# Performance work log

Hardware: AMD Instinct MI355X
Metric: run time of the kernel (lower is better)

The kernel has to match this reference:

```python
import jax, jax.numpy as jnp
import numpy as np

DIM = 1024
NUM_HEADS = 16
MASKED = True


def setup_inputs() -> dict:
    key = jax.random.key(0)
    ks = jax.random.split(key, 9)
    B, S, D = 2, 2048, DIM
    return {
        "x": jax.random.normal(ks[0], (B, S, D), dtype=jnp.float32),
        "Wq": jax.random.normal(ks[1], (D, D), dtype=jnp.float32),
        "bq": jax.random.normal(ks[2], (D,), dtype=jnp.float32),
        "Wk": jax.random.normal(ks[3], (D, D), dtype=jnp.float32),
        "bk": jax.random.normal(ks[4], (D,), dtype=jnp.float32),
        "Wv": jax.random.normal(ks[5], (D, D), dtype=jnp.float32),
        "bv": jax.random.normal(ks[6], (D,), dtype=jnp.float32),
        "Wo": jax.random.normal(ks[7], (D, D), dtype=jnp.float32),
        "bo": jax.random.normal(ks[8], (D,), dtype=jnp.float32),
    }


def _mha(x, Wq, bq, Wk, bk, Wv, bv, Wo, bo):
    B, S, D = x.shape
    H = NUM_HEADS
    hd = D // H
    # projections (torch Linear stores [out,in]; here W is [out,in], x @ W.T + b)
    q = x @ Wq.T + bq
    k = x @ Wk.T + bk
    v = x @ Wv.T + bv
    # [B, H, S, hd]
    q = q.reshape(B, S, H, hd).transpose(0, 2, 1, 3)
    k = k.reshape(B, S, H, hd).transpose(0, 2, 1, 3)
    v = v.reshape(B, S, H, hd).transpose(0, 2, 1, 3)
    scores = jnp.einsum("bhqd,bhkd->bhqk", q, k) / jnp.sqrt(jnp.asarray(hd, x.dtype))
    if MASKED:
        mask = jnp.tril(jnp.ones((S, S), dtype=bool))
        scores = jnp.where(mask, scores, -jnp.inf)
    attn = jax.nn.softmax(scores, axis=-1)
    out = jnp.einsum("bhqk,bhkd->bhqd", attn, v)
    out = out.transpose(0, 2, 1, 3).reshape(B, S, D)
    return out @ Wo.T + bo


def reference(x, Wq, bq, Wk, bk, Wv, bv, Wo, bo):
    return _mha(x, Wq, bq, Wk, bk, Wv, bv, Wo, bo)
```

## Files before the change

### kernel.cpp

```cpp
#include <hip/hip_runtime.h>

typedef unsigned short u16;
typedef unsigned int u32;
typedef __attribute__((ext_vector_type(4))) float f32x4;
typedef __attribute__((ext_vector_type(8))) __bf16 bf16x8;

#define L2E 1.4426950408889634f

__device__ __forceinline__ u16 f2bf(float f) { return __builtin_bit_cast(u16, (__bf16)f); }
__device__ __forceinline__ float bf2f(u16 h) { return (float)__builtin_bit_cast(__bf16, h); }
__device__ __forceinline__ f32x4 mfma16(bf16x8 a, bf16x8 b, f32x4 c) {
  return __builtin_amdgcn_mfma_f32_16x16x32_bf16(a, b, c, 0, 0, 0);
}
__device__ __forceinline__ void gl_lds16(const u16* g, u16* l) {
  __builtin_amdgcn_global_load_lds((__attribute__((address_space(1))) void*)g,
                                   (__attribute__((address_space(3))) void*)l,
                                   16, 0, 0);
}
__device__ __forceinline__ f32x4 fzero() {
  f32x4 v = {0.f, 0.f, 0.f, 0.f};
  return v;
}

__global__ void k_prep(const float* __restrict__ x, const float* __restrict__ Wq,
                       const float* __restrict__ Wk, const float* __restrict__ Wv,
                       const float* __restrict__ Wo,
                       u16* __restrict__ xh, u16* __restrict__ xl,
                       u16* __restrict__ wqh, u16* __restrict__ wql,
                       u16* __restrict__ wkh, u16* __restrict__ wkl,
                       u16* __restrict__ wvb, u16* __restrict__ wob) {
  int i = (blockIdx.x * 256 + threadIdx.x) * 4;
  const float* src;
  u16* hi;
  u16* lo;
  int j;
  if (i < 4194304)      { src = x;  hi = xh;  lo = xl;      j = i; }
  else if (i < 5242880) { src = Wq; hi = wqh; lo = wql;     j = i - 4194304; }
  else if (i < 6291456) { src = Wk; hi = wkh; lo = wkl;     j = i - 5242880; }
  else if (i < 7340032) { src = Wv; hi = wvb; lo = nullptr; j = i - 6291456; }
  else                  { src = Wo; hi = wob; lo = nullptr; j = i - 7340032; }
  float4 v = *(const float4*)(src + j);
  float vv[4] = {v.x, v.y, v.z, v.w};
  u16 hh[4];
#pragma unroll
  for (int t = 0; t < 4; ++t) hh[t] = f2bf(vv[t]);
  *(ushort4*)(hi + j) = make_ushort4(hh[0], hh[1], hh[2], hh[3]);
  if (lo) {
    u16 ll[4];
#pragma unroll
    for (int t = 0; t < 4; ++t) ll[t] = f2bf(vv[t] - bf2f(hh[t]));
    *(ushort4*)(lo + j) = make_ushort4(ll[0], ll[1], ll[2], ll[3]);
  }
}

template <int SPLIT, int EPI>
__device__ __forceinline__ void gemm_body(
    u16* sm, const u16* __restrict__ Ah, const u16* __restrict__ Al,
    const u16* __restrict__ Bh, const u16* __restrict__ Bl,
    const float* __restrict__ bias, float scale,
    u16* __restrict__ oH, u16* __restrict__ oL, float* __restrict__ oF,
    int m0, int n0) {
  u16* sAh = sm;
  u16* sBh = sm + 4096;
  u16* sAl = SPLIT ? (sm + 8192) : sm;
  u16* sBl = SPLIT ? (sm + 12288) : sm;

  const int tid = threadIdx.x;
  const int lane = tid & 63, w = tid >> 6;
  const int wm = w >> 1, wn = w & 1;
  const int fr = lane & 15, fg = lane >> 4;
  const int srow = tid >> 2, sblk = tid & 3;
  const int sswz = (sblk ^ (srow & 3)) * 8;
  const int sdst = sblk * 8;
  const int rswz = (fg ^ (fr & 3)) * 8;

  f32x4 acc[4][4];
#pragma unroll
  for (int i = 0; i < 4; ++i)
#pragma unroll
    for (int j = 0; j < 4; ++j) acc[i][j] = fzero();

  for (int kk = 0; kk < 1024; kk += 32) {
    __syncthreads();
#pragma unroll
    for (int r = 0; r < 2; ++r) {
      int row = r * 64 + srow;
      gl_lds16(Ah + (size_t)(m0 + row) * 1024 + kk + sswz, sAh + row * 32 + sdst);
      gl_lds16(Bh + (size_t)(n0 + row) * 1024 + kk + sswz, sBh + row * 32 + sdst);
      if constexpr (SPLIT) {
        gl_lds16(Al + (size_t)(m0 + row) * 1024 + kk + sswz, sAl + row * 32 + sdst);
        gl_lds16(Bl + (size_t)(n0 + row) * 1024 + kk + sswz, sBl + row * 32 + sdst);
      }
    }
    __syncthreads();

    bf16x8 ah[4], bh[4], al[4], bl[4];
#pragma unroll
    for (int i = 0; i < 4; ++i) {
      ah[i] = *(const bf16x8*)(sAh + (wm * 64 + i * 16 + fr) * 32 + rswz);
      bh[i] = *(const bf16x8*)(sBh + (wn * 64 + i * 16 + fr) * 32 + rswz);
      if constexpr (SPLIT) {
        al[i] = *(const bf16x8*)(sAl + (wm * 64 + i * 16 + fr) * 32 + rswz);
        bl[i] = *(const bf16x8*)(sBl + (wn * 64 + i * 16 + fr) * 32 + rswz);
      }
    }
#pragma unroll
    for (int i = 0; i < 4; ++i)
#pragma unroll
      for (int j = 0; j < 4; ++j) {
        acc[i][j] = mfma16(ah[i], bh[j], acc[i][j]);
        if constexpr (SPLIT) {
          acc[i][j] = mfma16(ah[i], bl[j], acc[i][j]);
          acc[i][j] = mfma16(al[i], bh[j], acc[i][j]);
        }
      }
  }

#pragma unroll
  for (int i = 0; i < 4; ++i)
#pragma unroll
    for (int j = 0; j < 4; ++j) {
      int cg = n0 + wn * 64 + j * 16 + fr;
      float bv = bias[cg];
      if constexpr (EPI == 1) {
        int rgb = m0 + wm * 64 + i * 16 + fg * 4;
        int b = rgb >> 11, s = rgb & 2047, hd2 = cg >> 6, dd = cg & 63;
        u16 hv[4];
#pragma unroll
        for (int r = 0; r < 4; ++r) hv[r] = f2bf((acc[i][j][r] + bv) * scale);
        *(ushort4*)(oH + ((size_t)((b * 16 + hd2) * 64 + dd)) * 2048 + s) =
            make_ushort4(hv[0], hv[1], hv[2], hv[3]);
      } else {
#pragma unroll
        for (int r = 0; r < 4; ++r) {
          int rg = m0 + wm * 64 + i * 16 + fg * 4 + r;
          float val = (acc[i][j][r] + bv) * scale;
          if constexpr (EPI == 0) {
            int b = rg >> 11, s = rg & 2047, hd2 = cg >> 6, dd = cg & 63;
            size_t off = ((size_t)((b * 16 + hd2) * 2048 + s)) * 64 + dd;
            u16 hv = f2bf(val);
            oH[off] = hv;
            oL[off] = f2bf(val - bf2f(hv));
          } else {
            oF[(size_t)rg * 1024 + cg] = val;
          }
        }
      }
    }
}

__global__ __launch_bounds__(256) void k_qkv(
    const u16* __restrict__ xh, const u16* __restrict__ xl,
    const u16* __restrict__ wqh, const u16* __restrict__ wql,
    const u16* __restrict__ wkh, const u16* __restrict__ wkl,
    const u16* __restrict__ wvb,
    const float* __restrict__ bq, const float* __restrict__ bk,
    const float* __restrict__ bv,
    u16* __restrict__ qh, u16* __restrict__ ql,
    u16* __restrict__ kh, u16* __restrict__ kl, u16* __restrict__ vt) {
  __shared__ u16 sm[16384];
  int which = blockIdx.y >> 3;
  int m0 = blockIdx.x * 128, n0 = (blockIdx.y & 7) * 128;
  if (which == 0)
    gemm_body<1, 0>(sm, xh, xl, wqh, wql, bq, 0.125f * L2E, qh, ql, nullptr, m0, n0);
  else if (which == 1)
    gemm_body<1, 0>(sm, xh, xl, wkh, wkl, bk, 1.0f, kh, kl, nullptr, m0, n0);
  else
    gemm_body<0, 1>(sm, xh, nullptr, wvb, nullptr, bv, 1.0f, vt, nullptr, nullptr, m0, n0);
}

__global__ __launch_bounds__(256) void k_oproj(
    const u16* __restrict__ A, const u16* __restrict__ B,
    const float* __restrict__ bias, float* __restrict__ out) {
  __shared__ u16 sm[6144];
  u16* sA = sm;
  u16* sB = sm + 2048;

  const int tid = threadIdx.x;
  const int lane = tid & 63, w = tid >> 6;
  const int fr = lane & 15, fg = lane >> 4;
  const int m0 = blockIdx.x * 64, n0 = blockIdx.y * 128;
  const int srow = tid >> 2, sblk = tid & 3;
  const int sswz = (sblk ^ (srow & 3)) * 8;
  const int sdst = sblk * 8;
  const int rswz = (fg ^ (fr & 3)) * 8;

  f32x4 acc[4][2];
#pragma unroll
  for (int i = 0; i < 4; ++i)
#pragma unroll
    for (int j = 0; j < 2; ++j) acc[i][j] = fzero();

  for (int kk = 0; kk < 1024; kk += 32) {
    __syncthreads();
    gl_lds16(A + (size_t)(m0 + srow) * 1024 + kk + sswz, sA + srow * 32 + sdst);
    gl_lds16(B + (size_t)(n0 + srow) * 1024 + kk + sswz, sB + srow * 32 + sdst);
    gl_lds16(B + (size_t)(n0 + 64 + srow) * 1024 + kk + sswz, sB + (64 + srow) * 32 + sdst);
    __syncthreads();

    bf16x8 af[4], bf_[2];
#pragma unroll
    for (int i = 0; i < 4; ++i)
      af[i] = *(const bf16x8*)(sA + (i * 16 + fr) * 32 + rswz);
#pragma unroll
    for (int j = 0; j < 2; ++j)
      bf_[j] = *(const bf16x8*)(sB + (w * 32 + j * 16 + fr) * 32 + rswz);
#pragma unroll
    for (int i = 0; i < 4; ++i)
#pragma unroll
      for (int j = 0; j < 2; ++j) acc[i][j] = mfma16(af[i], bf_[j], acc[i][j]);
  }

#pragma unroll
  for (int i = 0; i < 4; ++i)
#pragma unroll
    for (int j = 0; j < 2; ++j) {
      int cg = n0 + w * 32 + j * 16 + fr;
      float bv = bias[cg];
#pragma unroll
      for (int r = 0; r < 4; ++r) {
        int rg = m0 + i * 16 + fg * 4 + r;
        out[(size_t)rg * 1024 + cg] = acc[i][j][r] + bv;
      }
    }
}

__global__ __launch_bounds__(512) void k_attn(
    const u16* __restrict__ Qh, const u16* __restrict__ Ql,
    const u16* __restrict__ Kh, const u16* __restrict__ Kl,
    const u16* __restrict__ Vt, u16* __restrict__ Oa) {
  __shared__ u16 sKh[2][4096], sKl[2][4096], sVt[2][4096];
  __shared__ u16 sP[8][1024];

  const int tid = threadIdx.x;
  const int lane = tid & 63, w = tid >> 6;
  const int fr = lane & 15, fg = lane >> 4;

  const int d = blockIdx.x;
  const int g = d >> 3;
  const int bh = (d & 7) * 4 + (g & 3);
  const int pr = g >> 2;

  const size_t base = (size_t)bh * 131072;
  const u16* Qh_p = Qh + base;
  const u16* Ql_p = Ql + base;
  const u16* Kh_p = Kh + base;
  const u16* Kl_p = Kl + base;
  const u16* Vt_p = Vt + base;
  const int bb = bh >> 4, hh = bh & 15;

  const int srow8 = tid >> 3, scb8 = tid & 7;

  auto STAGE = [&](int t, int c) {
    int cbs = scb8 ^ (srow8 & 7);
    gl_lds16(Kh_p + ((size_t)(t * 64 + srow8)) * 64 + cbs * 8, &sKh[c][srow8 * 64 + scb8 * 8]);
    gl_lds16(Kl_p + ((size_t)(t * 64 + srow8)) * 64 + cbs * 8, &sKl[c][srow8 * 64 + scb8 * 8]);
    gl_lds16(Vt_p + (size_t)srow8 * 2048 + t * 64 + cbs * 8, &sVt[c][srow8 * 64 + scb8 * 8]);
  };

  for (int half = 0; half < 2; ++half) {
    const int j = half ? (15 - pr) : pr;
    const int nt = 2 * (j + 1);
    const int qrow = j * 128 + w * 16 + fr;

    bf16x8 qhf[2], qlf[2];
#pragma unroll
    for (int ks = 0; ks < 2; ++ks) {
      qhf[ks] = *(const bf16x8*)(Qh_p + (size_t)qrow * 64 + ks * 32 + fg * 8);
      qlf[ks] = *(const bf16x8*)(Ql_p + (size_t)qrow * 64 + ks * 32 + fg * 8);
    }

    float mx = -1e30f, l = 0.f;
    f32x4 o[4];
#pragma unroll
    for (int f = 0; f < 4; ++f) o[f] = fzero();

    STAGE(0, 0);

    for (int t = 0; t < nt; ++t) {
      const int cur = t & 1;
      if (t + 1 < nt) {
        STAGE(t + 1, cur ^ 1);
        asm volatile("s_waitcnt vmcnt(3)" ::: "memory");
      } else {
        asm volatile("s_waitcnt vmcnt(0)" ::: "memory");
      }
      asm volatile("s_barrier" ::: "memory");

      const u16* kbh = sKh[cur];
      const u16* kbl = sKl[cur];
      const u16* vbb = sVt[cur];

      f32x4 sc[4];
      __builtin_amdgcn_s_setprio(1);
#pragma unroll
      for (int f = 0; f < 4; ++f) {
        f32x4 a = fzero();
#pragma unroll
        for (int ks = 0; ks < 2; ++ks) {
          int row = f * 16 + fr;
          int cb = (fg + 4 * ks) ^ (fr & 7);
          bf16x8 khv = *(const bf16x8*)(kbh + row * 64 + cb * 8);
          bf16x8 klv = *(const bf16x8*)(kbl + row * 64 + cb * 8);
          a = mfma16(khv, qhf[ks], a);
          a = mfma16(khv, qlf[ks], a);
          a = mfma16(klv, qhf[ks], a);
        }
        sc[f] = a;
      }
      __builtin_amdgcn_s_setprio(0);

      if (t >= nt - 2) {
#pragma unroll
        for (int f = 0; f < 4; ++f)
#pragma unroll
          for (int r = 0; r < 4; ++r) {
            int kvg = t * 64 + f * 16 + fg * 4 + r;
            if (kvg > qrow) sc[f][r] = -1e30f;
          }
      }

      float pm = -1e30f;
#pragma unroll
      for (int f = 0; f < 4; ++f)
#pragma unroll
        for (int r = 0; r < 4; ++r) pm = fmaxf(pm, sc[f][r]);
      pm = fmaxf(pm, __shfl_xor(pm, 16, 64));
      pm = fmaxf(pm, __shfl_xor(pm, 32, 64));

      const bool resc = __any(pm > mx + 11.5f);
      float alp = 1.0f;
      if (resc) {
        float mn = fmaxf(mx, pm);
        alp = exp2f(mx - mn);
        mx = mn;
      }

      float ps = 0.f;
#pragma unroll
      for (int f = 0; f < 4; ++f) {
        float p0 = exp2f(sc[f][0] - mx);
        float p1 = exp2f(sc[f][1] - mx);
        float p2 = exp2f(sc[f][2] - mx);
        float p3 = exp2f(sc[f][3] - mx);
        ps += (p0 + p1) + (p2 + p3);
        uint2 pv;
        pv.x = (u32)f2bf(p0) | ((u32)f2bf(p1) << 16);
        pv.y = (u32)f2bf(p2) | ((u32)f2bf(p3) << 16);
        int e = (f * 16 + fg * 4) ^ ((fr & 7) << 3);
        *(uint2*)(&sP[w][fr * 64 + e]) = pv;
      }
      ps += __shfl_xor(ps, 16, 64);
      ps += __shfl_xor(ps, 32, 64);
      l = l * alp + ps;

      if (resc) {
        float alpb[4];
#pragma unroll
        for (int r = 0; r < 4; ++r) alpb[r] = __shfl(alp, fg * 4 + r, 64);
#pragma unroll
        for (int f = 0; f < 4; ++f)
#pragma unroll
          for (int r = 0; r < 4; ++r) o[f][r] *= alpb[r];
      }

      __builtin_amdgcn_s_setprio(1);
#pragma unroll
      for (int ks = 0; ks < 2; ++ks) {
        int e = (ks * 32 + fg * 8) ^ ((fr & 7) << 3);
        bf16x8 pa = *(const bf16x8*)(&sP[w][fr * 64 + e]);
#pragma unroll
        for (int f = 0; f < 4; ++f) {
          int row = f * 16 + fr;
          int cb = (fg + 4 * ks) ^ (fr & 7);
          bf16x8 vb = *(const bf16x8*)(vbb + row * 64 + cb * 8);
          o[f] = mfma16(pa, vb, o[f]);
        }
      }
      __builtin_amdgcn_s_setprio(0);

      asm volatile("s_barrier" ::: "memory");
    }

    float lb[4];
#pragma unroll
    for (int r = 0; r < 4; ++r) lb[r] = __shfl(l, fg * 4 + r, 64);
#pragma unroll
    for (int f = 0; f < 4; ++f)
#pragma unroll
      for (int r = 0; r < 4; ++r) {
        int qg = j * 128 + w * 16 + fg * 4 + r;
        float val = o[f][r] / lb[r];
        Oa[((size_t)(bb * 2048 + qg)) * 1024 + hh * 64 + f * 16 + fr] = f2bf(val);
      }
  }
}

extern "C" void kernel_launch(void* const* d_in, const int* in_sizes, int n_in,
                              void* d_out, int out_size, void* d_ws, size_t ws_size,
                              hipStream_t stream) {
  const float* x  = (const float*)d_in[0];
  const float* Wq = (const float*)d_in[1];
  const float* bq = (const float*)d_in[2];
  const float* Wk = (const float*)d_in[3];
  const float* bk = (const float*)d_in[4];
  const float* Wv = (const float*)d_in[5];
  const float* bv = (const float*)d_in[6];
  const float* Wo = (const float*)d_in[7];
  const float* bo = (const float*)d_in[8];
  float* out = (float*)d_out;

  u16* ws  = (u16*)d_ws;
  u16* xh  = ws;
  u16* xl  = xh + 4194304;
  u16* wqh = xl + 4194304;
  u16* wql = wqh + 1048576;
  u16* wkh = wql + 1048576;
  u16* wkl = wkh + 1048576;
  u16* wvb = wkl + 1048576;
  u16* wob = wvb + 1048576;
  u16* qh  = wob + 1048576;
  u16* ql  = qh + 4194304;
  u16* kh  = ql + 4194304;
  u16* kl  = kh + 4194304;
  u16* vt  = kl + 4194304;
  u16* ao  = xh;

  k_prep<<<8192, 256, 0, stream>>>(x, Wq, Wk, Wv, Wo, xh, xl, wqh, wql, wkh, wkl, wvb, wob);
  k_qkv<<<dim3(32, 24), 256, 0, stream>>>(xh, xl, wqh, wql, wkh, wkl, wvb, bq, bk, bv,
                                          qh, ql, kh, kl, vt);
  k_attn<<<256, 512, 0, stream>>>(qh, ql, kh, kl, vt, ao);
  k_oproj<<<dim3(64, 8), 256, 0, stream>>>(ao, wob, bo, out);
}
```

Before: 173.3 us.

## Double GEMM K-tile, remap QKV blocks per XCD, triple-buffer attention K/V

The QKV and output-projection GEMMs now stage 64-wide K tiles with a new XOR swizzle, which halves the barrier count per K. They also raise MFMA priority and add occupancy hints to launch_bounds. The QKV grid becomes 1D, with block indices remapped so blocks on the same XCD share M rows for L2 reuse. Attention moves to a three-deep K/V ring buffer, which drops the trailing barrier per tile and adds a barrier between halves. The costs are more LDS per block, which may lower occupancy, and some added risk of read-after-overwrite hazards in the ring buffer.

After: 154.7 us. 1.12x faster.

```diff
diff --git a/kernel.cpp b/kernel.cpp
--- a/kernel.cpp
+++ b/kernel.cpp
@@ -61,18 +61,16 @@
     u16* __restrict__ oH, u16* __restrict__ oL, float* __restrict__ oF,
     int m0, int n0) {
   u16* sAh = sm;
-  u16* sBh = sm + 4096;
-  u16* sAl = SPLIT ? (sm + 8192) : sm;
-  u16* sBl = SPLIT ? (sm + 12288) : sm;
+  u16* sBh = sm + 8192;
+  u16* sAl = SPLIT ? (sm + 16384) : sm;
+  u16* sBl = SPLIT ? (sm + 24576) : sm;
 
   const int tid = threadIdx.x;
   const int lane = tid & 63, w = tid >> 6;
   const int wm = w >> 1, wn = w & 1;
   const int fr = lane & 15, fg = lane >> 4;
-  const int srow = tid >> 2, sblk = tid & 3;
-  const int sswz = (sblk ^ (srow & 3)) * 8;
-  const int sdst = sblk * 8;
-  const int rswz = (fg ^ (fr & 3)) * 8;
+  const int strow = tid >> 3;
+  const int stcb = (tid & 7) * 16;
 
   f32x4 acc[4][4];
 #pragma unroll
@@ -80,40 +78,49 @@
 #pragma unroll
     for (int j = 0; j < 4; ++j) acc[i][j] = fzero();
 
-  for (int kk = 0; kk < 1024; kk += 32) {
+  for (int kk = 0; kk < 1024; kk += 64) {
     __syncthreads();
 #pragma unroll
-    for (int r = 0; r < 2; ++r) {
-      int row = r * 64 + srow;
-      gl_lds16(Ah + (size_t)(m0 + row) * 1024 + kk + sswz, sAh + row * 32 + sdst);
-      gl_lds16(Bh + (size_t)(n0 + row) * 1024 + kk + sswz, sBh + row * 32 + sdst);
+    for (int c = 0; c < 4; ++c) {
+      int row = c * 32 + strow;
+      int srcc = (stcb ^ (((row >> 2) & 1) << 5)) >> 1;
+      int dstc = row * 64 + (stcb >> 1);
+      gl_lds16(Ah + (size_t)(m0 + row) * 1024 + kk + srcc, sAh + dstc);
+      gl_lds16(Bh + (size_t)(n0 + row) * 1024 + kk + srcc, sBh + dstc);
       if constexpr (SPLIT) {
-        gl_lds16(Al + (size_t)(m0 + row) * 1024 + kk + sswz, sAl + row * 32 + sdst);
-        gl_lds16(Bl + (size_t)(n0 + row) * 1024 + kk + sswz, sBl + row * 32 + sdst);
+        gl_lds16(Al + (size_t)(m0 + row) * 1024 + kk + srcc, sAl + dstc);
+        gl_lds16(Bl + (size_t)(n0 + row) * 1024 + kk + srcc, sBl + dstc);
       }
     }
     __syncthreads();
 
-    bf16x8 ah[4], bh[4], al[4], bl[4];
-#pragma unroll
-    for (int i = 0; i < 4; ++i) {
-      ah[i] = *(const bf16x8*)(sAh + (wm * 64 + i * 16 + fr) * 32 + rswz);
-      bh[i] = *(const bf16x8*)(sBh + (wn * 64 + i * 16 + fr) * 32 + rswz);
-      if constexpr (SPLIT) {
-        al[i] = *(const bf16x8*)(sAl + (wm * 64 + i * 16 + fr) * 32 + rswz);
-        bl[i] = *(const bf16x8*)(sBl + (wn * 64 + i * 16 + fr) * 32 + rswz);
-      }
-    }
-#pragma unroll
-    for (int i = 0; i < 4; ++i)
-#pragma unroll
-      for (int j = 0; j < 4; ++j) {
-        acc[i][j] = mfma16(ah[i], bh[j], acc[i][j]);
-        if constexpr (SPLIT) {
-          acc[i][j] = mfma16(ah[i], bl[j], acc[i][j]);
-          acc[i][j] = mfma16(al[i], bh[j], acc[i][j]);
+#pragma unroll
+    for (int kk2 = 0; kk2 < 2; ++kk2) {
+      bf16x8 ah[4], bh[4], al[4], bl[4];
+#pragma unroll
+      for (int i = 0; i < 4; ++i) {
+        int ra = wm * 64 + i * 16 + fr;
+        int ca = (kk2 * 64 + fg * 16) ^ (((ra >> 2) & 1) << 5);
+        ah[i] = *(const bf16x8*)(sAh + ra * 64 + (ca >> 1));
+        if constexpr (SPLIT) al[i] = *(const bf16x8*)(sAl + ra * 64 + (ca >> 1));
+        int rb = wn * 64 + i * 16 + fr;
+        int cb = (kk2 * 64 + fg * 16) ^ (((rb >> 2) & 1) << 5);
+        bh[i] = *(const bf16x8*)(sBh + rb * 64 + (cb >> 1));
+        if constexpr (SPLIT) bl[i] = *(const bf16x8*)(sBl + rb * 64 + (cb >> 1));
+      }
+      __builtin_amdgcn_s_setprio(1);
+#pragma unroll
+      for (int i = 0; i < 4; ++i)
+#pragma unroll
+        for (int j = 0; j < 4; ++j) {
+          acc[i][j] = mfma16(ah[i], bh[j], acc[i][j]);
+          if constexpr (SPLIT) {
+            acc[i][j] = mfma16(ah[i], bl[j], acc[i][j]);
+            acc[i][j] = mfma16(al[i], bh[j], acc[i][j]);
+          }
         }
-      }
+      __builtin_amdgcn_s_setprio(0);
+    }
   }
 
 #pragma unroll
@@ -149,7 +156,7 @@
     }
 }
 
-__global__ __launch_bounds__(256) void k_qkv(
+__global__ __launch_bounds__(256, 2) void k_qkv(
     const u16* __restrict__ xh, const u16* __restrict__ xl,
     const u16* __restrict__ wqh, const u16* __restrict__ wql,
     const u16* __restrict__ wkh, const u16* __restrict__ wkl,
@@ -158,78 +165,99 @@
     const float* __restrict__ bv,
     u16* __restrict__ qh, u16* __restrict__ ql,
     u16* __restrict__ kh, u16* __restrict__ kl, u16* __restrict__ vt) {
-  __shared__ u16 sm[16384];
-  int which = blockIdx.y >> 3;
-  int m0 = blockIdx.x * 128, n0 = (blockIdx.y & 7) * 128;
-  if (which == 0)
+  __shared__ u16 sm[32768];
+  const int d = blockIdx.x;
+  const int xcd = d & 7, j = d >> 3;
+  const int m0 = (xcd * 4 + (j & 3)) * 128;
+  const int pn = j >> 2;
+  const int proj = pn >> 3, n0 = (pn & 7) * 128;
+  if (proj == 0)
     gemm_body<1, 0>(sm, xh, xl, wqh, wql, bq, 0.125f * L2E, qh, ql, nullptr, m0, n0);
-  else if (which == 1)
+  else if (proj == 1)
     gemm_body<1, 0>(sm, xh, xl, wkh, wkl, bk, 1.0f, kh, kl, nullptr, m0, n0);
   else
     gemm_body<0, 1>(sm, xh, nullptr, wvb, nullptr, bv, 1.0f, vt, nullptr, nullptr, m0, n0);
 }
 
-__global__ __launch_bounds__(256) void k_oproj(
+__global__ __launch_bounds__(256, 4) void k_oproj(
     const u16* __restrict__ A, const u16* __restrict__ B,
     const float* __restrict__ bias, float* __restrict__ out) {
-  __shared__ u16 sm[6144];
+  __shared__ u16 sm[12288];
   u16* sA = sm;
-  u16* sB = sm + 2048;
+  u16* sB = sm + 4096;
 
   const int tid = threadIdx.x;
   const int lane = tid & 63, w = tid >> 6;
   const int fr = lane & 15, fg = lane >> 4;
   const int m0 = blockIdx.x * 64, n0 = blockIdx.y * 128;
-  const int srow = tid >> 2, sblk = tid & 3;
-  const int sswz = (sblk ^ (srow & 3)) * 8;
-  const int sdst = sblk * 8;
-  const int rswz = (fg ^ (fr & 3)) * 8;
+  const int strow = tid >> 3;
+  const int stcb = (tid & 7) * 16;
 
   f32x4 acc[4][2];
 #pragma unroll
   for (int i = 0; i < 4; ++i)
 #pragma unroll
-    for (int j = 0; j < 2; ++j) acc[i][j] = fzero();
-
-  for (int kk = 0; kk < 1024; kk += 32) {
+    for (int jj = 0; jj < 2; ++jj) acc[i][jj] = fzero();
+
+  for (int kk = 0; kk < 1024; kk += 64) {
     __syncthreads();
-    gl_lds16(A + (size_t)(m0 + srow) * 1024 + kk + sswz, sA + srow * 32 + sdst);
-    gl_lds16(B + (size_t)(n0 + srow) * 1024 + kk + sswz, sB + srow * 32 + sdst);
-    gl_lds16(B + (size_t)(n0 + 64 + srow) * 1024 + kk + sswz, sB + (64 + srow) * 32 + sdst);
+#pragma unroll
+    for (int c = 0; c < 2; ++c) {
+      int row = c * 32 + strow;
+      int srcc = (stcb ^ (((row >> 2) & 1) << 5)) >> 1;
+      gl_lds16(A + (size_t)(m0 + row) * 1024 + kk + srcc, sA + row * 64 + (stcb >> 1));
+    }
+#pragma unroll
+    for (int c = 0; c < 4; ++c) {
+      int row = c * 32 + strow;
+      int srcc = (stcb ^ (((row >> 2) & 1) << 5)) >> 1;
+      gl_lds16(B + (size_t)(n0 + row) * 1024 + kk + srcc, sB + row * 64 + (stcb >> 1));
+    }
     __syncthreads();
 
-    bf16x8 af[4], bf_[2];
-#pragma unroll
-    for (int i = 0; i < 4; ++i)
-      af[i] = *(const bf16x8*)(sA + (i * 16 + fr) * 32 + rswz);
-#pragma unroll
-    for (int j = 0; j < 2; ++j)
-      bf_[j] = *(const bf16x8*)(sB + (w * 32 + j * 16 + fr) * 32 + rswz);
-#pragma unroll
-    for (int i = 0; i < 4; ++i)
-#pragma unroll
-      for (int j = 0; j < 2; ++j) acc[i][j] = mfma16(af[i], bf_[j], acc[i][j]);
+#pragma unroll
+    for (int kk2 = 0; kk2 < 2; ++kk2) {
+      bf16x8 af[4], bf_[2];
+#pragma unroll
+      for (int i = 0; i < 4; ++i) {
+        int ra = i * 16 + fr;
+        int ca = (kk2 * 64 + fg * 16) ^ (((ra >> 2) & 1) << 5);
+        af[i] = *(const bf16x8*)(sA + ra * 64 + (ca >> 1));
+      }
+#pragma unroll
+      for (int jj = 0; jj < 2; ++jj) {
+        int rb = w * 32 + jj * 16 + fr;
+        int cb = (kk2 * 64 + fg * 16) ^ (((rb >> 2) & 1) << 5);
+        bf_[jj] = *(const bf16x8*)(sB + rb * 64 + (cb >> 1));
+      }
+      __builtin_amdgcn_s_setprio(1);
+#pragma unroll
+      for (int i = 0; i < 4; ++i)
+#pragma unroll
+        for (int jj = 0; jj < 2; ++jj) acc[i][jj] = mfma16(af[i], bf_[jj], acc[i][jj]);
+      __builtin_amdgcn_s_setprio(0);
+    }
   }
 
 #pragma unroll
   for (int i = 0; i < 4; ++i)
 #pragma unroll
-    for (int j = 0; j < 2; ++j) {
-      int cg = n0 + w * 32 + j * 16 + fr;
+    for (int jj = 0; jj < 2; ++jj) {
+      int cg = n0 + w * 32 + jj * 16 + fr;
       float bv = bias[cg];
 #pragma unroll
       for (int r = 0; r < 4; ++r) {
         int rg = m0 + i * 16 + fg * 4 + r;
-        out[(size_t)rg * 1024 + cg] = acc[i][j][r] + bv;
-      }
-    }
-}
-
-__global__ __launch_bounds__(512) void k_attn(
+        out[(size_t)rg * 1024 + cg] = acc[i][jj][r] + bv;
+      }
+    }
+}
+
+__global__ __launch_bounds__(512, 2) void k_attn(
     const u16* __restrict__ Qh, const u16* __restrict__ Ql,
     const u16* __restrict__ Kh, const u16* __restrict__ Kl,
     const u16* __restrict__ Vt, u16* __restrict__ Oa) {
-  __shared__ u16 sKh[2][4096], sKl[2][4096], sVt[2][4096];
+  __shared__ u16 sKh[3][4096], sKl[3][4096], sVt[3][4096];
   __shared__ u16 sP[8][1024];
 
   const int tid = threadIdx.x;
@@ -263,6 +291,10 @@
     const int nt = 2 * (j + 1);
     const int qrow = j * 128 + w * 16 + fr;
 
+    if (half) asm volatile("s_barrier" ::: "memory");
+    int cur = 0;
+    STAGE(0, 0);
+
     bf16x8 qhf[2], qlf[2];
 #pragma unroll
     for (int ks = 0; ks < 2; ++ks) {
@@ -275,12 +307,11 @@
 #pragma unroll
     for (int f = 0; f < 4; ++f) o[f] = fzero();
 
-    STAGE(0, 0);
-
     for (int t = 0; t < nt; ++t) {
-      const int cur = t & 1;
+      int nxt = cur + 1;
+      if (nxt == 3) nxt = 0;
       if (t + 1 < nt) {
-        STAGE(t + 1, cur ^ 1);
+        STAGE(t + 1, nxt);
         asm volatile("s_waitcnt vmcnt(3)" ::: "memory");
       } else {
         asm volatile("s_waitcnt vmcnt(0)" ::: "memory");
@@ -379,7 +410,7 @@
       }
       __builtin_amdgcn_s_setprio(0);
 
-      asm volatile("s_barrier" ::: "memory");
+      cur = nxt;
     }
 
     float lb[4];
@@ -427,8 +458,8 @@
   u16* ao  = xh;
 
   k_prep<<<8192, 256, 0, stream>>>(x, Wq, Wk, Wv, Wo, xh, xl, wqh, wql, wkh, wkl, wvb, wob);
-  k_qkv<<<dim3(32, 24), 256, 0, stream>>>(xh, xl, wqh, wql, wkh, wkl, wvb, bq, bk, bv,
-                                          qh, ql, kh, kl, vt);
+  k_qkv<<<768, 256, 0, stream>>>(xh, xl, wqh, wql, wkh, wkl, wvb, bq, bk, bv,
+                                 qh, ql, kh, kl, vt);
   k_attn<<<256, 512, 0, stream>>>(qh, ql, kh, kl, vt, ao);
   k_oproj<<<dim3(64, 8), 256, 0, stream>>>(ao, wob, bo, out);
 }
```
